# Optimization experiments

Measured on AMD Instinct MI355X. Metric: run time of the kernel, lower is better.

The kernel has to match this reference:

```python
import jax, jax.numpy as jnp
import numpy as np

BN_EPS = 1e-5

def setup_inputs() -> dict:
    key = jax.random.key(0)
    B, C, T, N = 64, 1, 1024, 512
    weighted_fmri = jax.random.normal(key, (B, C, T, N), dtype=jnp.float32)
    bn_weight = jnp.ones((1,), dtype=jnp.float32)   # BatchNorm2d(1) affine weight
    bn_bias = jnp.zeros((1,), dtype=jnp.float32)    # BatchNorm2d(1) affine bias
    return {"weighted_fmri": weighted_fmri, "bn_weight": bn_weight, "bn_bias": bn_bias}


def reference(weighted_fmri, bn_weight, bn_bias):
    # weighted_fmri: [B, 1, T, N]. Original applies BatchNorm2d(1) per-sample
    # (batch of size 1 in training mode => normalize each sample by its own
    # mean/biased-var over (T, N)), then corrcoef over ROIs (columns).
    x = weighted_fmri
    mean = jnp.mean(x, axis=(1, 2, 3), keepdims=True)           # [B,1,1,1]
    var = jnp.mean((x - mean) ** 2, axis=(1, 2, 3), keepdims=True)  # biased var
    w = bn_weight.reshape(1, -1, 1, 1)
    b = bn_bias.reshape(1, -1, 1, 1)
    y = (x - mean) * jax.lax.rsqrt(var + BN_EPS) * w + b        # [B,1,T,N]

    X = y[:, 0]                                                 # [B,T,N]
    T = X.shape[1]
    # corrcoef(X.T): variables = N ROIs, observations = T timepoints
    Xc = X - jnp.mean(X, axis=1, keepdims=True)                 # center over time
    cov = jnp.einsum("btn,btm->bnm", Xc, Xc) / (T - 1)          # [B,N,N]
    d = jnp.sqrt(jnp.diagonal(cov, axis1=1, axis2=2))           # [B,N]
    corr = cov / (d[:, :, None] * d[:, None, :])
    return jnp.clip(corr, -1.0, 1.0)                            # [B,N,N]
```

## Files before the change

kernel.cpp:

```cpp
#include <hip/hip_runtime.h>

typedef __attribute__((ext_vector_type(8))) short bf16x8;
typedef __attribute__((ext_vector_type(4))) short s16x4;
typedef __attribute__((ext_vector_type(4))) float f32x4;

#define B_ 64
#define T_ 1024
#define N_ 512

__device__ __forceinline__ void async16(const void* g, void* l) {
  __builtin_amdgcn_global_load_lds(
      (const __attribute__((address_space(1))) unsigned int*)g,
      (__attribute__((address_space(3))) unsigned int*)l, 16, 0, 0);
}

__device__ __forceinline__ short f2bf(float f) {
  unsigned u = __builtin_bit_cast(unsigned, f);
  u += 0x7fffu + ((u >> 16) & 1u);
  return (short)(u >> 16);
}
__device__ __forceinline__ float bf2f(short s) {
  return __builtin_bit_cast(float, ((unsigned)(unsigned short)s) << 16);
}

__global__ __launch_bounds__(256, 4) void k_prep(
    const float* __restrict__ X, short* __restrict__ XbT,
    float* __restrict__ amu, float* __restrict__ invd)
{
  __shared__ __align__(16) short tile[64][68];
  const int b   = blockIdx.y;
  const int n0  = blockIdx.x * 64;
  const int tid = threadIdx.x;
  const int nch = tid & 15;
  const int rg  = tid >> 4;

  float s[4] = {0.f,0.f,0.f,0.f}, q[4] = {0.f,0.f,0.f,0.f};

  for (int tt = 0; tt < 16; ++tt) {
    const int t0 = tt * 64;
    #pragma unroll
    for (int i = 0; i < 4; ++i) {
      const int tr = rg + i * 16;
      const float4 v = *(const float4*)&X[((size_t)b*T_ + t0 + tr)*N_ + n0 + nch*4];
      short bb[4];
      bb[0] = f2bf(v.x); bb[1] = f2bf(v.y); bb[2] = f2bf(v.z); bb[3] = f2bf(v.w);
      #pragma unroll
      for (int c = 0; c < 4; ++c) { float f = bf2f(bb[c]); s[c] += f; q[c] += f*f; }
      s16x4 pk = { bb[0], bb[1], bb[2], bb[3] };
      *(s16x4*)&tile[tr][nch*4] = pk;
    }
    __syncthreads();
    #pragma unroll
    for (int i = 0; i < 4; ++i) {
      const int n = rg + i * 16;
      s16x4 o = { tile[nch*4+0][n], tile[nch*4+1][n],
                  tile[nch*4+2][n], tile[nch*4+3][n] };
      *(s16x4*)&XbT[((size_t)b*N_ + n0 + n)*T_ + t0 + nch*4] = o;
    }
    __syncthreads();
  }

  float* fb = (float*)&tile[0][0];
  #pragma unroll
  for (int c = 0; c < 4; ++c) { fb[tid*8 + c] = s[c]; fb[tid*8 + 4 + c] = q[c]; }
  __syncthreads();
  if (tid < 64) {
    const int qc = tid >> 2, c = tid & 3;
    float cs = 0.f, sq = 0.f;
    #pragma unroll
    for (int g = 0; g < 16; ++g) {
      cs += fb[(g*16 + qc)*8 + c];
      sq += fb[(g*16 + qc)*8 + 4 + c];
    }
    const int n = n0 + qc*4 + c;
    amu[b*N_ + n]  = cs * (1.f/32.f);
    invd[b*N_ + n] = rsqrtf(fmaxf(sq - cs*cs*(1.f/1024.f), 1e-20f));
  }
}

__global__ __launch_bounds__(256, 2) void k_gram(
    const short* __restrict__ XbT, const float* __restrict__ amu,
    const float* __restrict__ invd, float* __restrict__ out)
{
  __shared__ __align__(16) short ldsA[2][128][32];
  __shared__ __align__(16) short ldsB[2][128][32];

  const int bid = (blockIdx.x & 7) * 80 + (blockIdx.x >> 3);
  const int b = bid / 10;
  const int t = bid - b * 10;
  const int ip = (t >= 4) + (t >= 7) + (t >= 9);
  const int jp = ip + t - ((ip * (9 - ip)) >> 1);
  const int rowBase = ip * 128, colBase = jp * 128;
  const bool diag = (ip == jp);

  const int tid = threadIdx.x, lane = tid & 63, wave = tid >> 6;
  const int wr = wave >> 1, wc = wave & 1;
  const short* Xb = XbT + (size_t)b * N_ * T_;

  const int r0 = tid >> 2, cl = tid & 3;
  const int cg = cl ^ ((r0 >> 1) & 3);
  const size_t ga0 = (size_t)(rowBase + r0)      * T_ + cg * 8;
  const size_t ga1 = (size_t)(rowBase + r0 + 64) * T_ + cg * 8;
  const size_t gb0 = (size_t)(colBase + r0)      * T_ + cg * 8;
  const size_t gb1 = (size_t)(colBase + r0 + 64) * T_ + cg * 8;

  const int fr = lane & 15, kc = lane >> 4;
  const int swz = (kc ^ ((fr >> 1) & 3)) * 8;

  f32x4 acc[4][4] = {};

  #define STAGE(bufi, kb)                                                    \
    do {                                                                     \
      char* la_ = (char*)&ldsA[bufi][0][0];                                  \
      async16(Xb + ga0 + (kb), la_ + tid * 16);                              \
      async16(Xb + ga1 + (kb), la_ + (tid + 256) * 16);                      \
      if (!diag) {                                                           \
        char* lb_ = (char*)&ldsB[bufi][0][0];                                \
        async16(Xb + gb0 + (kb), lb_ + tid * 16);                            \
        async16(Xb + gb1 + (kb), lb_ + (tid + 256) * 16);                    \
      }                                                                      \
    } while (0)

  STAGE(0, 0);
  __syncthreads();
  int cur = 0;
  #pragma unroll 1
  for (int kt = 0; kt < 32; ++kt) {
    if (kt < 31) STAGE(cur ^ 1, (kt + 1) * 32);
    const short (*A)[32]  = ldsA[cur];
    const short (*Bm)[32] = diag ? ldsA[cur] : ldsB[cur];
    bf16x8 af[4], bfv[4];
    #pragma unroll
    for (int mi = 0; mi < 4; ++mi)
      af[mi] = *(const bf16x8*)&A[wr*64 + mi*16 + fr][swz];
    #pragma unroll
    for (int ni = 0; ni < 4; ++ni)
      bfv[ni] = *(const bf16x8*)&Bm[wc*64 + ni*16 + fr][swz];
    #pragma unroll
    for (int mi = 0; mi < 4; ++mi)
      #pragma unroll
      for (int ni = 0; ni < 4; ++ni)
        acc[mi][ni] = __builtin_amdgcn_mfma_f32_16x16x32_bf16(
            af[mi], bfv[ni], acc[mi][ni], 0, 0, 0);
    __syncthreads();
    cur ^= 1;
  }

  const int jc = colBase + wc * 64 + fr;
  float aj[4], dj[4];
  #pragma unroll
  for (int ni = 0; ni < 4; ++ni) {
    aj[ni] = amu[b*N_ + jc + ni*16];
    dj[ni] = invd[b*N_ + jc + ni*16];
  }
  #pragma unroll
  for (int mi = 0; mi < 4; ++mi) {
    const int ibase = rowBase + wr*64 + mi*16 + kc*4;
    float ai[4], di[4];
    #pragma unroll
    for (int r = 0; r < 4; ++r) {
      ai[r] = amu[b*N_ + ibase + r];
      di[r] = invd[b*N_ + ibase + r];
    }
    #pragma unroll
    for (int ni = 0; ni < 4; ++ni) {
      f32x4 g;
      #pragma unroll
      for (int r = 0; r < 4; ++r) {
        float v = (acc[mi][ni][r] - ai[r]*aj[ni]) * (di[r]*dj[ni]);
        g[r] = fminf(fmaxf(v, -1.f), 1.f);
      }
      const int J = jc + ni*16;
      #pragma unroll
      for (int r = 0; r < 4; ++r)
        out[((size_t)b*N_ + ibase + r)*N_ + J] = g[r];
      if (!diag)
        *(f32x4*)&out[((size_t)b*N_ + J)*N_ + ibase] = g;
    }
  }
}

extern "C" void kernel_launch(void* const* d_in, const int* in_sizes, int n_in,
                              void* d_out, int out_size, void* d_ws, size_t ws_size,
                              hipStream_t stream) {
  const float* X = (const float*)d_in[0];
  float* out = (float*)d_out;

  char* ws = (char*)d_ws;
  short* XbT  = (short*)ws;
  size_t off  = (size_t)B_ * N_ * T_ * sizeof(short);
  float* amu  = (float*)(ws + off);
  float* invd = amu + B_ * N_;

  k_prep<<<dim3(N_/64, B_), 256, 0, stream>>>(X, XbT, amu, invd);
  k_gram<<<dim3(64 * 10), 256, 0, stream>>>(XbT, amu, invd, out);
}
```

Before: 70.07 us.

## Give each wave a private LDS double-buffer pipeline instead of block-wide syncs

The block-shared A/B LDS tiles and per-iteration __syncthreads are replaced by per-wave private LDS buffers. Each wave loads its own 64-row A and B slices with global_load_lds and synchronises only with vmcnt/lgkmcnt waits, prefetching two stages ahead. MFMA sections run at raised priority via s_setprio. The aim is to remove block barriers and let waves progress independently, at the cost of redundant global loads across waves that share tiles, higher LDS use (64KB per block), and possible occupancy loss. The f2bf conversion is also switched to the library intrinsic.

New measurement: 78.99 us. 1.13x slower.

```diff
diff --git a/kernel.cpp b/kernel.cpp
--- a/kernel.cpp
+++ b/kernel.cpp
@@ -1,4 +1,5 @@
 #include <hip/hip_runtime.h>
+#include <hip/hip_bf16.h>
 
 typedef __attribute__((ext_vector_type(8))) short bf16x8;
 typedef __attribute__((ext_vector_type(4))) short s16x4;
@@ -7,6 +8,9 @@
 #define B_ 64
 #define T_ 1024
 #define N_ 512
+
+#define VMWAIT(N) asm volatile("s_waitcnt vmcnt(" #N ")" ::: "memory")
+#define LGKM0()   asm volatile("s_waitcnt lgkmcnt(0)" ::: "memory")
 
 __device__ __forceinline__ void async16(const void* g, void* l) {
   __builtin_amdgcn_global_load_lds(
@@ -15,9 +19,7 @@
 }
 
 __device__ __forceinline__ short f2bf(float f) {
-  unsigned u = __builtin_bit_cast(unsigned, f);
-  u += 0x7fffu + ((u >> 16) & 1u);
-  return (short)(u >> 16);
+  return __builtin_bit_cast(short, __float2bfloat16(f));
 }
 __device__ __forceinline__ float bf2f(short s) {
   return __builtin_bit_cast(float, ((unsigned)(unsigned short)s) << 16);
@@ -78,12 +80,60 @@
   }
 }
 
+template<int LPW>
+__device__ __forceinline__ void wave_pipeline(
+    const short* __restrict__ Xb, const size_t* gA, const size_t* gB,
+    short* ldsW, int lane, int aoffL, int boffL, f32x4 (&acc)[4][4])
+{
+  auto stg = [&](int buf, int kb) {
+    char* base = (char*)ldsW + buf * 8192;
+    #pragma unroll
+    for (int m = 0; m < 4; ++m)
+      async16(Xb + gA[m] + kb, base + m * 1024 + lane * 16);
+    if constexpr (LPW == 8) {
+      #pragma unroll
+      for (int m = 0; m < 4; ++m)
+        async16(Xb + gB[m] + kb, base + 4096 + m * 1024 + lane * 16);
+    }
+  };
+  auto body = [&](int buf, int kb_next, bool do_stg) {
+    const short* P = ldsW + buf * 4096;
+    bf16x8 af[4], bfv[4];
+    #pragma unroll
+    for (int mi = 0; mi < 4; ++mi) af[mi] = *(const bf16x8*)&P[aoffL + mi * 512];
+    #pragma unroll
+    for (int ni = 0; ni < 4; ++ni) bfv[ni] = *(const bf16x8*)&P[boffL + ni * 512];
+    LGKM0();
+    if (do_stg) stg(buf, kb_next);
+    __builtin_amdgcn_s_setprio(1);
+    #pragma unroll
+    for (int mi = 0; mi < 4; ++mi)
+      #pragma unroll
+      for (int ni = 0; ni < 4; ++ni)
+        acc[mi][ni] = __builtin_amdgcn_mfma_f32_16x16x32_bf16(
+            af[mi], bfv[ni], acc[mi][ni], 0, 0, 0);
+    __builtin_amdgcn_s_setprio(0);
+  };
+
+  stg(0, 0); stg(1, 32);
+  #pragma unroll 1
+  for (int t = 0; t < 30; t += 2) {
+    if constexpr (LPW == 8) VMWAIT(8); else VMWAIT(4);
+    body(0, (t + 2) * 32, true);
+    if constexpr (LPW == 8) VMWAIT(8); else VMWAIT(4);
+    body(1, (t + 3) * 32, true);
+  }
+  if constexpr (LPW == 8) VMWAIT(8); else VMWAIT(4);
+  body(0, 0, false);
+  VMWAIT(0);
+  body(1, 0, false);
+}
+
 __global__ __launch_bounds__(256, 2) void k_gram(
     const short* __restrict__ XbT, const float* __restrict__ amu,
     const float* __restrict__ invd, float* __restrict__ out)
 {
-  __shared__ __align__(16) short ldsA[2][128][32];
-  __shared__ __align__(16) short ldsB[2][128][32];
+  __shared__ __align__(16) short lds[4][8192];
 
   const int bid = (blockIdx.x & 7) * 80 + (blockIdx.x >> 3);
   const int b = bid / 10;
@@ -97,60 +147,33 @@
   const int wr = wave >> 1, wc = wave & 1;
   const short* Xb = XbT + (size_t)b * N_ * T_;
 
-  const int r0 = tid >> 2, cl = tid & 3;
-  const int cg = cl ^ ((r0 >> 1) & 3);
-  const size_t ga0 = (size_t)(rowBase + r0)      * T_ + cg * 8;
-  const size_t ga1 = (size_t)(rowBase + r0 + 64) * T_ + cg * 8;
-  const size_t gb0 = (size_t)(colBase + r0)      * T_ + cg * 8;
-  const size_t gb1 = (size_t)(colBase + r0 + 64) * T_ + cg * 8;
+  const int rowG = rowBase + wr * 64;
+  const int colG = colBase + wc * 64;
+  const bool dup = diag && (wr == wc);
+
+  size_t gA[4], gB[4];
+  #pragma unroll
+  for (int m = 0; m < 4; ++m) {
+    const int row = 16 * m + (lane >> 2);
+    const int cg  = (lane & 3) ^ ((row >> 1) & 3);
+    gA[m] = (size_t)(rowG + row) * T_ + cg * 8;
+    gB[m] = (size_t)(colG + row) * T_ + cg * 8;
+  }
 
   const int fr = lane & 15, kc = lane >> 4;
-  const int swz = (kc ^ ((fr >> 1) & 3)) * 8;
+  const int swz   = (kc ^ ((fr >> 1) & 3)) * 8;
+  const int aoffL = fr * 32 + swz;
+  const int boffL = (dup ? 0 : 2048) + fr * 32 + swz;
 
   f32x4 acc[4][4] = {};
-
-  #define STAGE(bufi, kb)                                                    \
-    do {                                                                     \
-      char* la_ = (char*)&ldsA[bufi][0][0];                                  \
-      async16(Xb + ga0 + (kb), la_ + tid * 16);                              \
-      async16(Xb + ga1 + (kb), la_ + (tid + 256) * 16);                      \
-      if (!diag) {                                                           \
-        char* lb_ = (char*)&ldsB[bufi][0][0];                                \
-        async16(Xb + gb0 + (kb), lb_ + tid * 16);                            \
-        async16(Xb + gb1 + (kb), lb_ + (tid + 256) * 16);                    \
-      }                                                                      \
-    } while (0)
-
-  STAGE(0, 0);
-  __syncthreads();
-  int cur = 0;
-  #pragma unroll 1
-  for (int kt = 0; kt < 32; ++kt) {
-    if (kt < 31) STAGE(cur ^ 1, (kt + 1) * 32);
-    const short (*A)[32]  = ldsA[cur];
-    const short (*Bm)[32] = diag ? ldsA[cur] : ldsB[cur];
-    bf16x8 af[4], bfv[4];
-    #pragma unroll
-    for (int mi = 0; mi < 4; ++mi)
-      af[mi] = *(const bf16x8*)&A[wr*64 + mi*16 + fr][swz];
-    #pragma unroll
-    for (int ni = 0; ni < 4; ++ni)
-      bfv[ni] = *(const bf16x8*)&Bm[wc*64 + ni*16 + fr][swz];
-    #pragma unroll
-    for (int mi = 0; mi < 4; ++mi)
-      #pragma unroll
-      for (int ni = 0; ni < 4; ++ni)
-        acc[mi][ni] = __builtin_amdgcn_mfma_f32_16x16x32_bf16(
-            af[mi], bfv[ni], acc[mi][ni], 0, 0, 0);
-    __syncthreads();
-    cur ^= 1;
-  }
+  if (dup) wave_pipeline<4>(Xb, gA, gB, &lds[wave][0], lane, aoffL, boffL, acc);
+  else     wave_pipeline<8>(Xb, gA, gB, &lds[wave][0], lane, aoffL, boffL, acc);
 
   const int jc = colBase + wc * 64 + fr;
   float aj[4], dj[4];
   #pragma unroll
   for (int ni = 0; ni < 4; ++ni) {
-    aj[ni] = amu[b*N_ + jc + ni*16];
+    aj[ni] = amu [b*N_ + jc + ni*16];
     dj[ni] = invd[b*N_ + jc + ni*16];
   }
   #pragma unroll
@@ -159,7 +182,7 @@
     float ai[4], di[4];
     #pragma unroll
     for (int r = 0; r < 4; ++r) {
-      ai[r] = amu[b*N_ + ibase + r];
+      ai[r] = amu [b*N_ + ibase + r];
       di[r] = invd[b*N_ + ibase + r];
     }
     #pragma unroll
@@ -170,7 +193,7 @@
         float v = (acc[mi][ni][r] - ai[r]*aj[ni]) * (di[r]*dj[ni]);
         g[r] = fminf(fmaxf(v, -1.f), 1.f);
       }
-      const int J = jc + ni*16;
+      const int J = jc + ni * 16;
       #pragma unroll
       for (int r = 0; r < 4; ++r)
         out[((size_t)b*N_ + ibase + r)*N_ + J] = g[r];
```
